# Optimization experiments

Hardware: AMD Instinct MI355X
Metric: run time of the kernel (lower is better)

The kernel has to match this reference:

```python
import jax, jax.numpy as jnp
import numpy as np

# Bayer pattern 'gbrg': 2x2 channel map (0=R,1=G,2=B)
#   (0,0)=G (0,1)=B
#   (1,0)=R (1,1)=G
CMAP = np.array([[1, 2], [0, 1]], dtype=np.int32)
XP = np.linspace(0.0, 255.0, 17).astype(np.float32)  # LUT knots

# 3x3 Gaussian blur kernel, sigma=0.4 (torchvision GaussianBlur)
def _gauss_kernel(sigma=0.4):
    x = np.array([-1.0, 0.0, 1.0], dtype=np.float32)
    g = np.exp(-(x ** 2) / (2.0 * sigma ** 2))
    g /= g.sum()
    return (g[:, None] * g[None, :]).astype(np.float32)

BLUR_K = _gauss_kernel()[None, None]  # [1,1,3,3]

# Malvar-He-Cutler demosaic kernels (/8)
_G_AT = np.array([[0,0,-1,0,0],[0,0,2,0,0],[-1,2,4,2,-1],[0,0,2,0,0],[0,0,-1,0,0]], np.float32) / 8.0
_K_H = np.array([[0,0,0.5,0,0],[0,-1,0,-1,0],[-1,4,5,4,-1],[0,-1,0,-1,0],[0,0,0.5,0,0]], np.float32) / 8.0
_K_V = _K_H.T.copy()
_K_D = np.array([[0,0,-1.5,0,0],[0,2,0,2,0],[-1.5,0,6,0,-1.5],[0,2,0,2,0],[0,0,-1.5,0,0]], np.float32) / 8.0
DEMOSAIC_K = np.stack([_G_AT, _K_H, _K_V, _K_D])[:, None]  # [4,1,5,5]


def _conv_reflect(x, k):
    p = k.shape[-1] // 2
    xp_ = jnp.pad(x, ((0, 0), (0, 0), (p, p), (p, p)), mode='reflect')
    return jax.lax.conv_general_dilated(xp_, jnp.asarray(k), (1, 1), 'VALID',
                                        dimension_numbers=('NCHW', 'OIHW', 'NCHW'))


def setup_inputs() -> dict:
    key = jax.random.key(0)
    k1, k2, k3, k4 = jax.random.split(key, 4)
    B, H, W = 32, 512, 512
    im = jax.random.uniform(k1, (B, 3, H, W), jnp.float32)           # normalized RGB
    yp = jnp.sort(jax.random.uniform(k2, (3, 17), jnp.float32) * 255.0, axis=1)  # per-channel calib curves
    sigma = 10.0 + 2.0 * jax.random.normal(k3, ())                   # N(noise_sigma, 2) draw
    noise = sigma * jax.random.normal(k4, (B, 1, H, W), jnp.float32)
    return {"im": im, "yp": yp, "noise": noise}


def reference(im, yp, noise):
    B, _, H, W = im.shape
    ys = jnp.arange(H) % 2
    xs = jnp.arange(W) % 2
    cmap = jnp.asarray(CMAP)[ys[:, None], xs[None, :]]               # [H,W] channel at each pixel

    im255 = im * 255.0
    # Mosaic: pick bayer channel at each pixel -> [B,1,H,W]
    bayer = jnp.take_along_axis(im255, cmap[None, None], axis=1)

    # Gaussian blur (reflect padding)
    blurred = _conv_reflect(bayer, BLUR_K)

    # Per-bayer-channel piecewise-linear calibration (np.interp semantics)
    xp_knots = jnp.asarray(XP)
    lin_r = jnp.interp(blurred, xp_knots, yp[0])
    lin_g = jnp.interp(blurred, xp_knots, yp[1])
    lin_b = jnp.interp(blurred, xp_knots, yp[2])
    c = cmap[None, None]
    linear = jnp.where(c == 0, lin_r, jnp.where(c == 1, lin_g, lin_b))

    # Additive noise
    noisy = linear + noise

    # Malvar demosaic: one 4-filter conv, then per-position selection
    f = _conv_reflect(noisy, DEMOSAIC_K)                             # [B,4,H,W]
    g_f, h_f, v_f, d_f = f[:, 0], f[:, 1], f[:, 2], f[:, 3]
    raw = noisy[:, 0]
    my = ys[:, None]
    mx = xs[None, :]
    p00 = (my == 0) & (mx == 0)   # G (blue row, red col)
    p01 = (my == 0) & (mx == 1)   # B
    p10 = (my == 1) & (mx == 0)   # R
    p11 = (my == 1) & (mx == 1)   # G (red row, blue col)

    R = jnp.where(p10, raw, jnp.where(p11, h_f, jnp.where(p00, v_f, d_f)))
    G = jnp.where(p00 | p11, raw, g_f)
    Bc = jnp.where(p01, raw, jnp.where(p00, h_f, jnp.where(p11, v_f, d_f)))
    rgb = jnp.stack([R, G, Bc], axis=1)                              # [B,3,H,W]

    return jnp.clip(rgb / 255.0, 0.0, 1.0)
```

## Files before the change

### kernel.cpp

```cpp
#include <hip/hip_runtime.h>


#define TDS 8

typedef float f4u __attribute__((ext_vector_type(4), aligned(16)));

struct HB { float hb0, hb1, hb2, hb3, hh0, hh1; };

__device__ __forceinline__ int refl(int i, int n) {
    return i < 0 ? -i : (i >= n ? 2 * n - 2 - i : i);
}

__device__ __forceinline__ float clip01(float x) {
    return fminf(fmaxf(x * (1.0f / 255.0f), 0.0f), 1.0f);
}

__global__ __launch_bounds__(256, 4) void camera_kernel(
    const float* __restrict__ im, const float* __restrict__ yp,
    const float* __restrict__ noise, float* __restrict__ out,
    int H, int W)
{
    __shared__ float2 s_tab[4][48];

    const int tid  = threadIdx.x;
    const int wv   = tid >> 6;
    const int lane = tid & 63;
    const int b    = blockIdx.z;

    const int stripes = W >> 8;
    const int slot    = blockIdx.x * 4 + wv;
    const int stripe  = slot % stripes;
    const int gy0     = (slot / stripes) * TDS;
    const int gx0     = stripe << 8;
    const int x0      = gx0 + 4 * lane;

    const size_t HW = (size_t)H * W;
    const float* p0  = im + (size_t)b * 3 * HW;
    const float* p1  = p0 + HW;
    const float* nzb = noise + (size_t)b * HW;

    if (lane < 48) {
        int ch = lane >> 4, i = lane & 15;
        s_tab[wv][lane] = make_float2(yp[ch * 17 + i], yp[ch * 17 + i + 1]);
    }
    asm volatile("s_waitcnt lgkmcnt(0)" ::: "memory");
    const float2* tabw = s_tab[wv];

    const bool l0   = (lane == 0), l63 = (lane == 63);
    const bool lInt = l0  && (gx0 != 0);
    const bool rInt = l63 && (x0 + 4 != W);
    const bool eInt = lInt || rInt;
    const bool eAny = l0 || l63;
    const int  xe   = l0 ? x0 - 4 : x0 + 4;
    const int  xen  = l0 ? x0 - 2 : x0 + 4;

    const float g0 = 0.04038794f;
    const float g1 = 0.91922413f;

    auto itp = [&](float tv, int ch) -> float {
        float s = tv * 16.0f;
        int i = (int)s; i = i < 0 ? 0 : (i > 15 ? 15 : i);
        float2 p = tabw[ch * 16 + i];
        return fmaf(s - (float)i, p.y - p.x, p.x);
    };

    auto mosrow = [&](int t) -> HB {
        int yr = refl(t, H);
        const float* pe = (t & 1) ? p0 : p1;
        const float* re = pe + (size_t)yr * W;
        const float* ro = re + HW;
        f4u a  = *(const f4u*)(re + x0);
        f4u bq = *(const f4u*)(ro + x0);
        float m0 = a.x, m1 = bq.y, m2 = a.z, m3 = bq.w;
        float ml = __shfl_up(m3, 1, 64);
        float mr = __shfl_down(m0, 1, 64);
        float me0 = 0.f, me1 = 0.f, me2 = 0.f, me3 = 0.f;
        if (eInt) {
            f4u ae = *(const f4u*)(re + xe);
            f4u be = *(const f4u*)(ro + xe);
            me0 = ae.x; me1 = be.y; me2 = ae.z; me3 = be.w;
        }
        if (l0)  ml = lInt ? me3 : m1;
        if (l63) mr = rInt ? me0 : m2;
        HB h;
        h.hb0 = fmaf(g0, ml + m1, g1 * m0);
        h.hb1 = fmaf(g0, m0 + m2, g1 * m1);
        h.hb2 = fmaf(g0, m1 + m3, g1 * m2);
        h.hb3 = fmaf(g0, m2 + mr, g1 * m3);
        float hL0 = fmaf(g0, me1 + me3, g1 * me2);
        float hL1 = fmaf(g0, me2 + m0,  g1 * me3);
        float hR0 = fmaf(g0, m3 + me1,  g1 * me0);
        float hR1 = fmaf(g0, me0 + me2, g1 * me1);
        h.hh0 = l0 ? hL0 : hR0;
        h.hh1 = l0 ? hL1 : hR1;
        return h;
    };

    float ring[5][8];
    HB hA = mosrow(gy0 - 3);
    HB hB = mosrow(gy0 - 2);
    const size_t outb = (size_t)b * 3 * HW;

    #pragma unroll
    for (int k = 0; k < TDS + 4; ++k) {
        const int r = gy0 - 2 + k;
        HB hC = mosrow(r + 1);
        float tb0 = fmaf(g0, hA.hb0 + hC.hb0, g1 * hB.hb0);
        float tb1 = fmaf(g0, hA.hb1 + hC.hb1, g1 * hB.hb1);
        float tb2 = fmaf(g0, hA.hb2 + hC.hb2, g1 * hB.hb2);
        float tb3 = fmaf(g0, hA.hb3 + hC.hb3, g1 * hB.hb3);
        float th0 = fmaf(g0, hA.hh0 + hC.hh0, g1 * hB.hh0);
        float th1 = fmaf(g0, hA.hh1 + hC.hh1, g1 * hB.hh1);
        const int chE = (k & 1) ? 0 : 1;
        const int chO = chE + 1;
        float c0 = itp(tb0, chE), c1 = itp(tb1, chO);
        float c2 = itp(tb2, chE), c3 = itp(tb3, chO);
        int yr = refl(r, H);
        const float* nzr = nzb + (size_t)yr * W;
        f4u nz = *(const f4u*)(nzr + x0);
        float2 nze = make_float2(0.f, 0.f);
        if (eInt) nze = *(const float2*)(nzr + xen);
        c0 += nz.x; c1 += nz.y; c2 += nz.z; c3 += nz.w;
        float e0 = 0.f, e1 = 0.f;
        if (eAny) { e0 = itp(th0, chE) + nze.x; e1 = itp(th1, chO) + nze.y; }
        float hl0 = __shfl_up(c2, 1, 64);
        float hl1 = __shfl_up(c3, 1, 64);
        float hr0 = __shfl_down(c0, 1, 64);
        float hr1 = __shfl_down(c1, 1, 64);
        if (l0)  { hl0 = lInt ? e0 : c2;  hl1 = lInt ? e1 : c1; }
        if (l63) { hr0 = rInt ? e0 : c2;  hr1 = rInt ? e1 : c1; }
        ring[k % 5][0] = hl0; ring[k % 5][1] = hl1;
        ring[k % 5][2] = c0;  ring[k % 5][3] = c1;
        ring[k % 5][4] = c2;  ring[k % 5][5] = c3;
        ring[k % 5][6] = hr0; ring[k % 5][7] = hr1;
        hA = hB; hB = hC;

        if (k >= 4) {
            const int y = gy0 + k - 4;
            float Rv[4], Gv[4], Bv[4];
            #pragma unroll
            for (int j = 0; j < 4; ++j) {
                const int cj = 2 + j;
                float c    = ring[(k - 2) % 5][cj];
                float ax1x = ring[(k - 2) % 5][cj - 1] + ring[(k - 2) % 5][cj + 1];
                float ax2x = ring[(k - 2) % 5][cj - 2] + ring[(k - 2) % 5][cj + 2];
                float ax1y = ring[(k - 3) % 5][cj] + ring[(k - 1) % 5][cj];
                float diag = ring[(k - 3) % 5][cj - 1] + ring[(k - 3) % 5][cj + 1]
                           + ring[(k - 1) % 5][cj - 1] + ring[(k - 1) % 5][cj + 1];
                float ax2y = ring[(k - 4) % 5][cj] + ring[k % 5][cj];
                const bool xO = (j & 1) != 0;
                const bool yO = (k & 1) != 0;
                float R, G, Bc;
                if (!yO && !xO) {
                    float hh = (0.5f * ax2y - diag - ax2x + 4.f * ax1x + 5.f * c) * 0.125f;
                    float vv = (0.5f * ax2x - diag - ax2y + 4.f * ax1y + 5.f * c) * 0.125f;
                    R = vv; G = c; Bc = hh;
                } else if (!yO && xO) {
                    float gg = (2.f * (ax1y + ax1x) - ax2y - ax2x + 4.f * c) * 0.125f;
                    float dd = (2.f * diag - 1.5f * (ax2y + ax2x) + 6.f * c) * 0.125f;
                    R = dd; G = gg; Bc = c;
                } else if (yO && !xO) {
                    float gg = (2.f * (ax1y + ax1x) - ax2y - ax2x + 4.f * c) * 0.125f;
                    float dd = (2.f * diag - 1.5f * (ax2y + ax2x) + 6.f * c) * 0.125f;
                    R = c; G = gg; Bc = dd;
                } else {
                    float hh = (0.5f * ax2y - diag - ax2x + 4.f * ax1x + 5.f * c) * 0.125f;
                    float vv = (0.5f * ax2x - diag - ax2y + 4.f * ax1y + 5.f * c) * 0.125f;
                    R = hh; G = c; Bc = vv;
                }
                Rv[j] = clip01(R); Gv[j] = clip01(G); Bv[j] = clip01(Bc);
            }
            size_t o = outb + (size_t)y * W + x0;
            *(f4u*)(out + o)          = (f4u){Rv[0], Rv[1], Rv[2], Rv[3]};
            *(f4u*)(out + o + HW)     = (f4u){Gv[0], Gv[1], Gv[2], Gv[3]};
            *(f4u*)(out + o + 2 * HW) = (f4u){Bv[0], Bv[1], Bv[2], Bv[3]};
        }
    }
}

extern "C" void kernel_launch(void* const* d_in, const int* in_sizes, int n_in,
                              void* d_out, int out_size, void* d_ws, size_t ws_size,
                              hipStream_t stream) {
    const float* im    = (const float*)d_in[0];
    const float* yp    = (const float*)d_in[1];
    const float* noise = (const float*)d_in[2];
    float* out = (float*)d_out;

    const int H = 512, W = 512;
    const int B = in_sizes[2] / (H * W);

    const int stripes = W / 256;
    const int slots   = stripes * (H / TDS);
    dim3 grid(slots / 4, 1, B);
    camera_kernel<<<grid, 256, 0, stream>>>(im, yp, noise, out, H, W);
}
```

Baseline: 45.22 us.

## Replace cross-lane shuffles with redundant per-lane halo loads for blur and demosaic

Each lane now loads a 12-pixel mosaic window (three float4s per parity row) and an 8-wide noise window, then computes its own blur and interpolation for the halo columns instead of exchanging neighbours via __shfl_up/down. Image-edge reflection is handled by remapping within the loaded window. This removes the shuffles and the lane-0/63 special-case loads and branches, but triples mosaic load instructions per lane (mostly L1/L2 hits) and doubles the interpolation work to 8 values per lane.

```diff
diff --git a/kernel.cpp b/kernel.cpp
--- a/kernel.cpp
+++ b/kernel.cpp
@@ -3,9 +3,8 @@
 
 #define TDS 8
 
-typedef float f4u __attribute__((ext_vector_type(4), aligned(16)));
-
-struct HB { float hb0, hb1, hb2, hb3, hh0, hh1; };
+typedef float f4a __attribute__((ext_vector_type(4), aligned(16)));
+typedef float f4b __attribute__((ext_vector_type(4), aligned(8)));
 
 __device__ __forceinline__ int refl(int i, int n) {
     return i < 0 ? -i : (i >= n ? 2 * n - 2 - i : i);
@@ -46,13 +45,9 @@
     asm volatile("s_waitcnt lgkmcnt(0)" ::: "memory");
     const float2* tabw = s_tab[wv];
 
-    const bool l0   = (lane == 0), l63 = (lane == 63);
-    const bool lInt = l0  && (gx0 != 0);
-    const bool rInt = l63 && (x0 + 4 != W);
-    const bool eInt = lInt || rInt;
-    const bool eAny = l0 || l63;
-    const int  xe   = l0 ? x0 - 4 : x0 + 4;
-    const int  xen  = l0 ? x0 - 2 : x0 + 4;
+    const int mcase = (x0 == 0) ? -1 : ((x0 == W - 4) ? 1 : 0);
+    const int cb    = (mcase < 0) ? 0 : ((mcase > 0) ? W - 12 : x0 - 4);
+    const int nb    = (mcase < 0) ? 0 : ((mcase > 0) ? W - 8  : x0 - 2);
 
     const float g0 = 0.04038794f;
     const float g1 = 0.91922413f;
@@ -64,76 +59,76 @@
         return fmaf(s - (float)i, p.y - p.x, p.x);
     };
 
-    auto mosrow = [&](int t) -> HB {
+    auto mosrow = [&](int t, float (&hb)[8]) {
         int yr = refl(t, H);
         const float* pe = (t & 1) ? p0 : p1;
         const float* re = pe + (size_t)yr * W;
         const float* ro = re + HW;
-        f4u a  = *(const f4u*)(re + x0);
-        f4u bq = *(const f4u*)(ro + x0);
-        float m0 = a.x, m1 = bq.y, m2 = a.z, m3 = bq.w;
-        float ml = __shfl_up(m3, 1, 64);
-        float mr = __shfl_down(m0, 1, 64);
-        float me0 = 0.f, me1 = 0.f, me2 = 0.f, me3 = 0.f;
-        if (eInt) {
-            f4u ae = *(const f4u*)(re + xe);
-            f4u be = *(const f4u*)(ro + xe);
-            me0 = ae.x; me1 = be.y; me2 = ae.z; me3 = be.w;
+        f4a e0 = *(const f4a*)(re + cb);
+        f4a e1 = *(const f4a*)(re + cb + 4);
+        f4a e2 = *(const f4a*)(re + cb + 8);
+        f4a q0 = *(const f4a*)(ro + cb);
+        f4a q1 = *(const f4a*)(ro + cb + 4);
+        f4a q2 = *(const f4a*)(ro + cb + 8);
+        float v[12] = {e0.x, q0.y, e0.z, q0.w, e1.x, q1.y, e1.z, q1.w,
+                       e2.x, q2.y, e2.z, q2.w};
+        float m[12];
+        if (mcase == 0) {
+            #pragma unroll
+            for (int j = 0; j < 12; ++j) m[j] = v[j];
+        } else if (mcase < 0) {
+            m[0] = v[4]; m[1] = v[3]; m[2] = v[2]; m[3] = v[1];
+            m[4] = v[0]; m[5] = v[1]; m[6] = v[2]; m[7] = v[3];
+            m[8] = v[4]; m[9] = v[5]; m[10] = v[6]; m[11] = v[7];
+        } else {
+            m[0] = v[4]; m[1] = v[5]; m[2] = v[6]; m[3] = v[7];
+            m[4] = v[8]; m[5] = v[9]; m[6] = v[10]; m[7] = v[11];
+            m[8] = v[10]; m[9] = v[9]; m[10] = v[8]; m[11] = v[7];
         }
-        if (l0)  ml = lInt ? me3 : m1;
-        if (l63) mr = rInt ? me0 : m2;
-        HB h;
-        h.hb0 = fmaf(g0, ml + m1, g1 * m0);
-        h.hb1 = fmaf(g0, m0 + m2, g1 * m1);
-        h.hb2 = fmaf(g0, m1 + m3, g1 * m2);
-        h.hb3 = fmaf(g0, m2 + mr, g1 * m3);
-        float hL0 = fmaf(g0, me1 + me3, g1 * me2);
-        float hL1 = fmaf(g0, me2 + m0,  g1 * me3);
-        float hR0 = fmaf(g0, m3 + me1,  g1 * me0);
-        float hR1 = fmaf(g0, me0 + me2, g1 * me1);
-        h.hh0 = l0 ? hL0 : hR0;
-        h.hh1 = l0 ? hL1 : hR1;
-        return h;
+        #pragma unroll
+        for (int j = 0; j < 8; ++j)
+            hb[j] = fmaf(g0, m[j + 1] + m[j + 3], g1 * m[j + 2]);
     };
 
     float ring[5][8];
-    HB hA = mosrow(gy0 - 3);
-    HB hB = mosrow(gy0 - 2);
+    float hrow[3][8];
+    mosrow(gy0 - 3, hrow[0]);
+    mosrow(gy0 - 2, hrow[1]);
     const size_t outb = (size_t)b * 3 * HW;
 
     #pragma unroll
     for (int k = 0; k < TDS + 4; ++k) {
         const int r = gy0 - 2 + k;
-        HB hC = mosrow(r + 1);
-        float tb0 = fmaf(g0, hA.hb0 + hC.hb0, g1 * hB.hb0);
-        float tb1 = fmaf(g0, hA.hb1 + hC.hb1, g1 * hB.hb1);
-        float tb2 = fmaf(g0, hA.hb2 + hC.hb2, g1 * hB.hb2);
-        float tb3 = fmaf(g0, hA.hb3 + hC.hb3, g1 * hB.hb3);
-        float th0 = fmaf(g0, hA.hh0 + hC.hh0, g1 * hB.hh0);
-        float th1 = fmaf(g0, hA.hh1 + hC.hh1, g1 * hB.hh1);
-        const int chE = (k & 1) ? 0 : 1;
-        const int chO = chE + 1;
-        float c0 = itp(tb0, chE), c1 = itp(tb1, chO);
-        float c2 = itp(tb2, chE), c3 = itp(tb3, chO);
+        mosrow(r + 1, hrow[(k + 2) % 3]);
+        const float* hA = hrow[k % 3];
+        const float* hB = hrow[(k + 1) % 3];
+        const float* hC = hrow[(k + 2) % 3];
+
         int yr = refl(r, H);
         const float* nzr = nzb + (size_t)yr * W;
-        f4u nz = *(const f4u*)(nzr + x0);
-        float2 nze = make_float2(0.f, 0.f);
-        if (eInt) nze = *(const float2*)(nzr + xen);
-        c0 += nz.x; c1 += nz.y; c2 += nz.z; c3 += nz.w;
-        float e0 = 0.f, e1 = 0.f;
-        if (eAny) { e0 = itp(th0, chE) + nze.x; e1 = itp(th1, chO) + nze.y; }
-        float hl0 = __shfl_up(c2, 1, 64);
-        float hl1 = __shfl_up(c3, 1, 64);
-        float hr0 = __shfl_down(c0, 1, 64);
-        float hr1 = __shfl_down(c1, 1, 64);
-        if (l0)  { hl0 = lInt ? e0 : c2;  hl1 = lInt ? e1 : c1; }
-        if (l63) { hr0 = rInt ? e0 : c2;  hr1 = rInt ? e1 : c1; }
-        ring[k % 5][0] = hl0; ring[k % 5][1] = hl1;
-        ring[k % 5][2] = c0;  ring[k % 5][3] = c1;
-        ring[k % 5][4] = c2;  ring[k % 5][5] = c3;
-        ring[k % 5][6] = hr0; ring[k % 5][7] = hr1;
-        hA = hB; hB = hC;
+        f4b zlo = *(const f4b*)(nzr + nb);
+        f4b zhi = *(const f4b*)(nzr + nb + 4);
+        float nv[8] = {zlo.x, zlo.y, zlo.z, zlo.w, zhi.x, zhi.y, zhi.z, zhi.w};
+        float n[8];
+        if (mcase == 0) {
+            #pragma unroll
+            for (int j = 0; j < 8; ++j) n[j] = nv[j];
+        } else if (mcase < 0) {
+            n[0] = nv[2]; n[1] = nv[1];
+            #pragma unroll
+            for (int j = 2; j < 8; ++j) n[j] = nv[j - 2];
+        } else {
+            #pragma unroll
+            for (int j = 0; j < 6; ++j) n[j] = nv[j + 2];
+            n[6] = nv[6]; n[7] = nv[5];
+        }
+
+        const int chE = (k & 1) ? 0 : 1;
+        #pragma unroll
+        for (int j = 0; j < 8; ++j) {
+            float tb = fmaf(g0, hA[j] + hC[j], g1 * hB[j]);
+            ring[k % 5][j] = itp(tb, (j & 1) ? chE + 1 : chE) + n[j];
+        }
 
         if (k >= 4) {
             const int y = gy0 + k - 4;
@@ -171,9 +166,9 @@
                 Rv[j] = clip01(R); Gv[j] = clip01(G); Bv[j] = clip01(Bc);
             }
             size_t o = outb + (size_t)y * W + x0;
-            *(f4u*)(out + o)          = (f4u){Rv[0], Rv[1], Rv[2], Rv[3]};
-            *(f4u*)(out + o + HW)     = (f4u){Gv[0], Gv[1], Gv[2], Gv[3]};
-            *(f4u*)(out + o + 2 * HW) = (f4u){Bv[0], Bv[1], Bv[2], Bv[3]};
+            *(f4a*)(out + o)          = (f4a){Rv[0], Rv[1], Rv[2], Rv[3]};
+            *(f4a*)(out + o + HW)     = (f4a){Gv[0], Gv[1], Gv[2], Gv[3]};
+            *(f4a*)(out + o + 2 * HW) = (f4a){Bv[0], Bv[1], Bv[2], Bv[3]};
         }
     }
 }
```

Result: slower. 69.25 us (+53.2%).
